# Performance work log

Measured on AMD Instinct MI355X. Metric: run time of the kernel, lower is better.

Reference implementation:

```python
import jax, jax.numpy as jnp
import numpy as np

T, N = 512, 256          # timesteps, parallel envs
STATE, HID = 64, 128     # input features, GRU hidden size


def setup_inputs() -> dict:
    key = jax.random.key(0)
    k = jax.random.split(key, 6)
    inputs = jax.random.normal(k[0], (T * N, STATE), dtype=jnp.float32)
    hxs = jax.random.normal(k[1], (N, HID), dtype=jnp.float32)
    masks = (jax.random.uniform(k[2], (T * N, 1)) > 0.02).astype(jnp.float32)
    # GRU params (torch layout: gates ordered r, z, n; rows = 3*HID)
    weight_ih = jax.random.normal(k[3], (3 * HID, STATE), dtype=jnp.float32) * 0.1
    weight_hh = jax.random.normal(k[4], (3 * HID, HID), dtype=jnp.float32) * 0.1
    bias_ih = jnp.zeros((3 * HID,), dtype=jnp.float32)  # init.constant_(0)
    bias_hh = jnp.zeros((3 * HID,), dtype=jnp.float32)
    return {
        "inputs": inputs, "hxs": hxs, "masks": masks,
        "weight_ih": weight_ih, "weight_hh": weight_hh,
        "bias_ih": bias_ih, "bias_hh": bias_hh,
    }


def reference(inputs, hxs, masks, weight_ih, weight_hh, bias_ih, bias_hh):
    n, hid = hxs.shape
    t = inputs.shape[0] // n
    x = inputs.reshape(t, n, -1)       # (t, n, state)
    m = masks.reshape(t, n, 1)         # (t, n, 1)

    # Input-to-gate projections are mask-independent: precompute for all steps.
    gx = jnp.einsum('tns,gs->tng', x, weight_ih) + bias_ih  # (t, n, 3H)

    def step(h, xs):
        gx_t, m_t = xs
        h = h * m_t                                 # inline reset (fused; replaces chunk splitting)
        gh = h @ weight_hh.T + bias_hh              # (n, 3H)
        xr, xz, xn = jnp.split(gx_t, 3, axis=-1)
        hr, hz, hn = jnp.split(gh, 3, axis=-1)
        r = jax.nn.sigmoid(xr + hr)
        z = jax.nn.sigmoid(xz + hz)
        cand = jnp.tanh(xn + r * hn)
        h = (1.0 - z) * cand + z * h                # torch GRU update
        return h, h

    h_final, ys = jax.lax.scan(step, hxs, (gx, m))  # ys: (t, n, H)
    return ys.reshape(t * n, hid), h_final
```

## Files before the change

kernel.cpp:

```cpp
#include <hip/hip_runtime.h>
#include <math.h>

#define T_STEPS  512
#define N_ENVS   256
#define STATE    64
#define HID      128
#define NTHREADS 512
#define XPAD     72

typedef _Float16 half8   __attribute__((ext_vector_type(8)));
typedef _Float16 half4_t __attribute__((ext_vector_type(4)));
typedef float    floatx4 __attribute__((ext_vector_type(4)));

#define BAR() asm volatile("s_waitcnt lgkmcnt(0)\n\ts_barrier" ::: "memory")

__device__ __forceinline__ float fexp2(float v) {
    float r;
    asm("v_exp_f32 %0, %1" : "=v"(r) : "v"(v));
    return r;
}
__device__ __forceinline__ float fexp2_nabs(float v) {
    float r;
    asm("v_exp_f32 %0, -|%1|" : "=v"(r) : "v"(v));
    return r;
}

__global__ __launch_bounds__(NTHREADS, 2) void gru_r12(
    const float* __restrict__ x,
    const float* __restrict__ h0,
    const float* __restrict__ masks,
    const float* __restrict__ wih,
    const float* __restrict__ whh,
    const float* __restrict__ bih,
    const float* __restrict__ bhh,
    float* __restrict__ out)
{
    const int b    = blockIdx.x;
    const int tid  = threadIdx.x;
    const int w    = tid >> 6;
    const int lane = tid & 63;
    const int c    = lane & 15;
    const int quad = lane >> 4;
    const int j    = 16 * w + c;

    __shared__ __align__(16) _Float16 buf[2][HID];
    __shared__ __align__(16) _Float16 xh[2][16][XPAD];
    __shared__ __align__(16) float    gxp[16][HID][4];

    const float SRZ = -1.44269504088896341f;
    const float SN  = -2.88539008177792681f;
    const float scl[3] = { SRZ, SRZ, SN };

    const int rowb[3] = { j, HID + j, 2 * HID + j };
    half8 Bh[3][4];
#pragma unroll
    for (int ti = 0; ti < 3; ++ti) {
        const int g = rowb[ti];
        const float sc = scl[ti];
#pragma unroll
        for (int kt = 0; kt < 4; ++kt) {
            const float* src = whh + (size_t)g * HID + kt * 32 + quad * 8;
            const float4 p0 = *(const float4*)(src);
            const float4 p1 = *(const float4*)(src + 4);
            half8 hb;
            hb[0] = (_Float16)(sc * p0.x); hb[1] = (_Float16)(sc * p0.y);
            hb[2] = (_Float16)(sc * p0.z); hb[3] = (_Float16)(sc * p0.w);
            hb[4] = (_Float16)(sc * p1.x); hb[5] = (_Float16)(sc * p1.y);
            hb[6] = (_Float16)(sc * p1.z); hb[7] = (_Float16)(sc * p1.w);
            Bh[ti][kt] = hb;
        }
    }
    half8 Bx[3][2];
#pragma unroll
    for (int ti = 0; ti < 3; ++ti) {
        const int g = rowb[ti];
        const float sc = scl[ti];
#pragma unroll
        for (int kt = 0; kt < 2; ++kt) {
            const float* src = wih + (size_t)g * STATE + kt * 32 + quad * 8;
            const float4 p0 = *(const float4*)(src);
            const float4 p1 = *(const float4*)(src + 4);
            half8 hb;
            hb[0] = (_Float16)(sc * p0.x); hb[1] = (_Float16)(sc * p0.y);
            hb[2] = (_Float16)(sc * p0.z); hb[3] = (_Float16)(sc * p0.w);
            hb[4] = (_Float16)(sc * p1.x); hb[5] = (_Float16)(sc * p1.y);
            hb[6] = (_Float16)(sc * p1.z); hb[7] = (_Float16)(sc * p1.w);
            Bx[ti][kt] = hb;
        }
    }

    const float br  = SRZ * (bih[j] + bhh[j]);
    const float bz  = SRZ * (bih[HID + j] + bhh[HID + j]);
    const float bxn = SN  * bih[2 * HID + j];
    const float bhn = SN  * bhh[2 * HID + j];

    const floatx4 zero4 = {0.f, 0.f, 0.f, 0.f};
    floatx4 cbhn = zero4; cbhn[0] = bhn;

    float hr = h0[(size_t)b * HID + j];
    float hm = masks[b] * hr;
    if (quad == 0) buf[0][j] = (_Float16)hm;

    float4 xp = {0.f, 0.f, 0.f, 0.f};
    if (tid < 256) {
        const int k = tid >> 4, cc = (tid & 15) * 4;
        const float4 xv = *(const float4*)(x + ((size_t)k * N_ENVS + b) * STATE + cc);
        half4_t hx = {(_Float16)xv.x, (_Float16)xv.y, (_Float16)xv.z, (_Float16)xv.w};
        *(half4_t*)&xh[0][k][cc] = hx;
        xp = *(const float4*)(x + ((size_t)(16 + k) * N_ENVS + b) * STATE + cc);
    }
    float mwin     = masks[(size_t)(1  + (lane & 15)) * N_ENVS + b];
    float mwin_nxt = masks[(size_t)(17 + (lane & 15)) * N_ENVS + b];

    float o[4] = {0.f, 0.f, 0.f, 0.f};

    floatx4 xg0, xg1, xg2;
    half8 axp0, axp1;

    BAR();

    {
        const _Float16* xr = &xh[0][c][0];
        half8 ax0 = *(const half8*)&xr[quad * 8];
        half8 ax1 = *(const half8*)&xr[32 + quad * 8];
        floatx4 g0 = __builtin_amdgcn_mfma_f32_16x16x32_f16(ax0, Bx[0][0], zero4, 0, 0, 0);
        floatx4 g1 = __builtin_amdgcn_mfma_f32_16x16x32_f16(ax0, Bx[1][0], zero4, 0, 0, 0);
        floatx4 g2 = __builtin_amdgcn_mfma_f32_16x16x32_f16(ax0, Bx[2][0], zero4, 0, 0, 0);
        g0 = __builtin_amdgcn_mfma_f32_16x16x32_f16(ax1, Bx[0][1], g0, 0, 0, 0);
        g1 = __builtin_amdgcn_mfma_f32_16x16x32_f16(ax1, Bx[1][1], g1, 0, 0, 0);
        g2 = __builtin_amdgcn_mfma_f32_16x16x32_f16(ax1, Bx[2][1], g2, 0, 0, 0);
#pragma unroll
        for (int i = 0; i < 4; ++i) {
            floatx4 p;
            p[0] = g0[i] + br;
            p[1] = g1[i] + bz;
            p[2] = g2[i] + bxn;
            p[3] = 0.f;
            *(floatx4*)&gxp[quad * 4 + i][j][0] = p;
        }
    }

    for (int tc = 0; tc < 32; ++tc) {
        if (tc > 0) {
            const int tbp = (tc - 1) * 16;
#pragma unroll
            for (int i = 0; i < 4; ++i)
                out[((size_t)(tbp + quad * 4 + i) * N_ENVS + b) * HID + j] = o[i];
            mwin = mwin_nxt;
            const int stm = (tc + 1) * 16 + 1 + (lane & 15);
            mwin_nxt = masks[(size_t)(stm < T_STEPS ? stm : T_STEPS - 1) * N_ENVS + b];
#pragma unroll
            for (int i = 0; i < 4; ++i) {
                floatx4 p;
                p[0] = xg0[i] + br;
                p[1] = xg1[i] + bz;
                p[2] = xg2[i] + bxn;
                p[3] = 0.f;
                *(floatx4*)&gxp[quad * 4 + i][j][0] = p;
            }
        }
        if (tid < 256) {
            const int k = tid >> 4, cc = (tid & 15) * 4;
            half4_t hx = {(_Float16)xp.x, (_Float16)xp.y, (_Float16)xp.z, (_Float16)xp.w};
            *(half4_t*)&xh[(tc + 1) & 1][k][cc] = hx;
            const int st = (tc + 2) * 16 + k;
            if (st < T_STEPS)
                xp = *(const float4*)(x + ((size_t)st * N_ENVS + b) * STATE + cc);
        }
        BAR();

#pragma unroll
        for (int s = 0; s < 16; ++s) {
            const _Float16* bufc = buf[s & 1];
            _Float16* bufn = (_Float16*)buf[(s + 1) & 1];

            half8 a0 = *(const half8*)(bufc + 0 * 32 + quad * 8);
            half8 a1 = *(const half8*)(bufc + 1 * 32 + quad * 8);
            half8 a2 = *(const half8*)(bufc + 2 * 32 + quad * 8);
            half8 a3 = *(const half8*)(bufc + 3 * 32 + quad * 8);
            const floatx4 gxh = *(const floatx4*)&gxp[s][j][0];
            const float mn = __int_as_float(__builtin_amdgcn_readlane(__float_as_int(mwin), s));

            if (s == 0) {
                const _Float16* xr = &xh[(tc + 1) & 1][c][0];
                axp0 = *(const half8*)&xr[quad * 8];
                axp1 = *(const half8*)&xr[32 + quad * 8];
            }

            floatx4 r_a = __builtin_amdgcn_mfma_f32_16x16x32_f16(a0, Bh[0][0], zero4, 0, 0, 0);
            floatx4 r_b = __builtin_amdgcn_mfma_f32_16x16x32_f16(a2, Bh[0][2], zero4, 0, 0, 0);
            floatx4 z_a = __builtin_amdgcn_mfma_f32_16x16x32_f16(a0, Bh[1][0], zero4, 0, 0, 0);
            floatx4 z_b = __builtin_amdgcn_mfma_f32_16x16x32_f16(a2, Bh[1][2], zero4, 0, 0, 0);
            floatx4 n_a = __builtin_amdgcn_mfma_f32_16x16x32_f16(a0, Bh[2][0], cbhn,  0, 0, 0);
            floatx4 n_b = __builtin_amdgcn_mfma_f32_16x16x32_f16(a2, Bh[2][2], zero4, 0, 0, 0);
            r_a = __builtin_amdgcn_mfma_f32_16x16x32_f16(a1, Bh[0][1], r_a, 0, 0, 0);
            r_b = __builtin_amdgcn_mfma_f32_16x16x32_f16(a3, Bh[0][3], r_b, 0, 0, 0);
            z_a = __builtin_amdgcn_mfma_f32_16x16x32_f16(a1, Bh[1][1], z_a, 0, 0, 0);
            z_b = __builtin_amdgcn_mfma_f32_16x16x32_f16(a3, Bh[1][3], z_b, 0, 0, 0);
            n_a = __builtin_amdgcn_mfma_f32_16x16x32_f16(a1, Bh[2][1], n_a, 0, 0, 0);
            n_b = __builtin_amdgcn_mfma_f32_16x16x32_f16(a3, Bh[2][3], n_b, 0, 0, 0);

            if (s == 1) xg0 = __builtin_amdgcn_mfma_f32_16x16x32_f16(axp0, Bx[0][0], zero4, 0, 0, 0);
            if (s == 2) xg1 = __builtin_amdgcn_mfma_f32_16x16x32_f16(axp0, Bx[1][0], zero4, 0, 0, 0);
            if (s == 3) xg2 = __builtin_amdgcn_mfma_f32_16x16x32_f16(axp0, Bx[2][0], zero4, 0, 0, 0);
            if (s == 4) xg0 = __builtin_amdgcn_mfma_f32_16x16x32_f16(axp1, Bx[0][1], xg0, 0, 0, 0);
            if (s == 5) xg1 = __builtin_amdgcn_mfma_f32_16x16x32_f16(axp1, Bx[1][1], xg1, 0, 0, 0);
            if (s == 6) xg2 = __builtin_amdgcn_mfma_f32_16x16x32_f16(axp1, Bx[2][1], xg2, 0, 0, 0);

            const float urp = (r_a[0] + r_b[0]) + gxh[0];
            const float uzp = (z_a[0] + z_b[0]) + gxh[1];
            const float hnp = n_a[0] + n_b[0];
            const float xnp = gxh[2];

            const float e_r = fexp2(urp);
            const float rg  = __builtin_amdgcn_rcpf(1.f + e_r);
            const float ap  = fmaf(rg, hnp, xnp);
            const float e_t = fexp2_nabs(ap);
            const float e_z = fexp2(fminf(uzp, 43.28f));
            const float opt = 1.f + e_t;
            const float num = fmaf(hm, opt, -copysignf(e_z * (1.f - e_t), ap));
            const float hnew = num * __builtin_amdgcn_rcpf(opt * (1.f + e_z));

            hm = mn * hnew;
            if (quad == 0) bufn[j] = (_Float16)hm;
            o[s & 3] = (quad == (s >> 2)) ? hnew : o[s & 3];
            if (s == 15) hr = hnew;
            BAR();
        }
    }

    {
        const int tbp = 31 * 16;
#pragma unroll
        for (int i = 0; i < 4; ++i)
            out[((size_t)(tbp + quad * 4 + i) * N_ENVS + b) * HID + j] = o[i];
    }
    if (quad == 0)
        out[(size_t)T_STEPS * N_ENVS * HID + (size_t)b * HID + j] = hr;
}

extern "C" void kernel_launch(void* const* d_in, const int* in_sizes, int n_in,
                              void* d_out, int out_size, void* d_ws, size_t ws_size,
                              hipStream_t stream) {
    const float* x   = (const float*)d_in[0];
    const float* h0  = (const float*)d_in[1];
    const float* mk  = (const float*)d_in[2];
    const float* wih = (const float*)d_in[3];
    const float* whh = (const float*)d_in[4];
    const float* bih = (const float*)d_in[5];
    const float* bhh = (const float*)d_in[6];
    float* out = (float*)d_out;

    hipLaunchKernelGGL(gru_r12, dim3(N_ENVS), dim3(NTHREADS), 0, stream,
                       x, h0, mk, wih, whh, bih, bhh, out);
}
```

Baseline: 281.9 us.

## Apply reset mask after the recurrent matmul and batch input projection per chunk

The mask multiply moves off the critical path. The unmasked hidden state is written to shared memory, and the mask scales the recurrent matmul results through fmaf, so the next step's MFMA does not wait on the mask multiply. The bias for the n gate is added in that fmaf rather than seeded into the MFMA accumulator. The input-projection MFMAs, previously spread across steps 1-6, now run as one batch at each chunk boundary. This shortens the per-step dependency chain but adds a burst of MFMA work between chunks.

New measurement: 280.2 us. About the same (-0.6%).

```diff
diff --git a/kernel.cpp b/kernel.cpp
--- a/kernel.cpp
+++ b/kernel.cpp
@@ -25,7 +25,7 @@
     return r;
 }
 
-__global__ __launch_bounds__(NTHREADS, 2) void gru_r12(
+__global__ __launch_bounds__(NTHREADS, 2) void gru_r13(
     const float* __restrict__ x,
     const float* __restrict__ h0,
     const float* __restrict__ masks,
@@ -95,11 +95,9 @@
     const float bhn = SN  * bhh[2 * HID + j];
 
     const floatx4 zero4 = {0.f, 0.f, 0.f, 0.f};
-    floatx4 cbhn = zero4; cbhn[0] = bhn;
 
     float hr = h0[(size_t)b * HID + j];
-    float hm = masks[b] * hr;
-    if (quad == 0) buf[0][j] = (_Float16)hm;
+    if (quad == 0) buf[0][j] = (_Float16)hr;
 
     float4 xp = {0.f, 0.f, 0.f, 0.f};
     if (tid < 256) {
@@ -109,12 +107,11 @@
         *(half4_t*)&xh[0][k][cc] = hx;
         xp = *(const float4*)(x + ((size_t)(16 + k) * N_ENVS + b) * STATE + cc);
     }
-    float mwin     = masks[(size_t)(1  + (lane & 15)) * N_ENVS + b];
-    float mwin_nxt = masks[(size_t)(17 + (lane & 15)) * N_ENVS + b];
+    float mwin     = masks[(size_t)((lane & 15)) * N_ENVS + b];
+    float mwin_nxt = masks[(size_t)(16 + (lane & 15)) * N_ENVS + b];
 
     float o[4] = {0.f, 0.f, 0.f, 0.f};
 
-    floatx4 xg0, xg1, xg2;
     half8 axp0, axp1;
 
     BAR();
@@ -147,14 +144,20 @@
             for (int i = 0; i < 4; ++i)
                 out[((size_t)(tbp + quad * 4 + i) * N_ENVS + b) * HID + j] = o[i];
             mwin = mwin_nxt;
-            const int stm = (tc + 1) * 16 + 1 + (lane & 15);
+            const int stm = (tc + 1) * 16 + (lane & 15);
             mwin_nxt = masks[(size_t)(stm < T_STEPS ? stm : T_STEPS - 1) * N_ENVS + b];
+            floatx4 g0 = __builtin_amdgcn_mfma_f32_16x16x32_f16(axp0, Bx[0][0], zero4, 0, 0, 0);
+            floatx4 g1 = __builtin_amdgcn_mfma_f32_16x16x32_f16(axp0, Bx[1][0], zero4, 0, 0, 0);
+            floatx4 g2 = __builtin_amdgcn_mfma_f32_16x16x32_f16(axp0, Bx[2][0], zero4, 0, 0, 0);
+            g0 = __builtin_amdgcn_mfma_f32_16x16x32_f16(axp1, Bx[0][1], g0, 0, 0, 0);
+            g1 = __builtin_amdgcn_mfma_f32_16x16x32_f16(axp1, Bx[1][1], g1, 0, 0, 0);
+            g2 = __builtin_amdgcn_mfma_f32_16x16x32_f16(axp1, Bx[2][1], g2, 0, 0, 0);
 #pragma unroll
             for (int i = 0; i < 4; ++i) {
                 floatx4 p;
-                p[0] = xg0[i] + br;
-                p[1] = xg1[i] + bz;
-                p[2] = xg2[i] + bxn;
+                p[0] = g0[i] + br;
+                p[1] = g1[i] + bz;
+                p[2] = g2[i] + bxn;
                 p[3] = 0.f;
                 *(floatx4*)&gxp[quad * 4 + i][j][0] = p;
             }
@@ -180,8 +183,9 @@
             half8 a3 = *(const half8*)(bufc + 3 * 32 + quad * 8);
             const floatx4 gxh = *(const floatx4*)&gxp[s][j][0];
             const float mn = __int_as_float(__builtin_amdgcn_readlane(__float_as_int(mwin), s));
-
-            if (s == 0) {
+            const float hm = mn * hr;
+
+            if (s == 15) {
                 const _Float16* xr = &xh[(tc + 1) & 1][c][0];
                 axp0 = *(const half8*)&xr[quad * 8];
                 axp1 = *(const half8*)&xr[32 + quad * 8];
@@ -191,7 +195,7 @@
             floatx4 r_b = __builtin_amdgcn_mfma_f32_16x16x32_f16(a2, Bh[0][2], zero4, 0, 0, 0);
             floatx4 z_a = __builtin_amdgcn_mfma_f32_16x16x32_f16(a0, Bh[1][0], zero4, 0, 0, 0);
             floatx4 z_b = __builtin_amdgcn_mfma_f32_16x16x32_f16(a2, Bh[1][2], zero4, 0, 0, 0);
-            floatx4 n_a = __builtin_amdgcn_mfma_f32_16x16x32_f16(a0, Bh[2][0], cbhn,  0, 0, 0);
+            floatx4 n_a = __builtin_amdgcn_mfma_f32_16x16x32_f16(a0, Bh[2][0], zero4, 0, 0, 0);
             floatx4 n_b = __builtin_amdgcn_mfma_f32_16x16x32_f16(a2, Bh[2][2], zero4, 0, 0, 0);
             r_a = __builtin_amdgcn_mfma_f32_16x16x32_f16(a1, Bh[0][1], r_a, 0, 0, 0);
             r_b = __builtin_amdgcn_mfma_f32_16x16x32_f16(a3, Bh[0][3], r_b, 0, 0, 0);
@@ -200,16 +204,9 @@
             n_a = __builtin_amdgcn_mfma_f32_16x16x32_f16(a1, Bh[2][1], n_a, 0, 0, 0);
             n_b = __builtin_amdgcn_mfma_f32_16x16x32_f16(a3, Bh[2][3], n_b, 0, 0, 0);
 
-            if (s == 1) xg0 = __builtin_amdgcn_mfma_f32_16x16x32_f16(axp0, Bx[0][0], zero4, 0, 0, 0);
-            if (s == 2) xg1 = __builtin_amdgcn_mfma_f32_16x16x32_f16(axp0, Bx[1][0], zero4, 0, 0, 0);
-            if (s == 3) xg2 = __builtin_amdgcn_mfma_f32_16x16x32_f16(axp0, Bx[2][0], zero4, 0, 0, 0);
-            if (s == 4) xg0 = __builtin_amdgcn_mfma_f32_16x16x32_f16(axp1, Bx[0][1], xg0, 0, 0, 0);
-            if (s == 5) xg1 = __builtin_amdgcn_mfma_f32_16x16x32_f16(axp1, Bx[1][1], xg1, 0, 0, 0);
-            if (s == 6) xg2 = __builtin_amdgcn_mfma_f32_16x16x32_f16(axp1, Bx[2][1], xg2, 0, 0, 0);
-
-            const float urp = (r_a[0] + r_b[0]) + gxh[0];
-            const float uzp = (z_a[0] + z_b[0]) + gxh[1];
-            const float hnp = n_a[0] + n_b[0];
+            const float urp = fmaf(mn, r_a[0] + r_b[0], gxh[0]);
+            const float uzp = fmaf(mn, z_a[0] + z_b[0], gxh[1]);
+            const float hnp = fmaf(mn, n_a[0] + n_b[0], bhn);
             const float xnp = gxh[2];
 
             const float e_r = fexp2(urp);
@@ -221,10 +218,9 @@
             const float num = fmaf(hm, opt, -copysignf(e_z * (1.f - e_t), ap));
             const float hnew = num * __builtin_amdgcn_rcpf(opt * (1.f + e_z));
 
-            hm = mn * hnew;
-            if (quad == 0) bufn[j] = (_Float16)hm;
+            if (quad == 0) bufn[j] = (_Float16)hnew;
             o[s & 3] = (quad == (s >> 2)) ? hnew : o[s & 3];
-            if (s == 15) hr = hnew;
+            hr = hnew;
             BAR();
         }
     }
@@ -251,6 +247,6 @@
     const float* bhh = (const float*)d_in[6];
     float* out = (float*)d_out;
 
-    hipLaunchKernelGGL(gru_r12, dim3(N_ENVS), dim3(NTHREADS), 0, stream,
+    hipLaunchKernelGGL(gru_r13, dim3(N_ENVS), dim3(NTHREADS), 0, stream,
                        x, h0, mk, wih, whh, bih, bhh, out);
 }
```
